# Performance work log

Measured on AMD Instinct MI355X. Metric: run time of the kernel, lower is better.

Reference implementation:

```python
import jax, jax.numpy as jnp
import numpy as np

N, E, H, IN_DIM, EDGE_DIM = 100000, 1600000, 64, 1, 1
SLOPE = 0.01  # leaky_relu negative slope (torch default; GATConv negative_slope=0.01)


def _lrelu(v):
    return jax.nn.leaky_relu(v, SLOPE)


def _segment_softmax(a, idx, num_segments):
    a_max = jax.ops.segment_max(a, idx, num_segments=num_segments)
    e = jnp.exp(a - a_max[idx])
    denom = jax.ops.segment_sum(e, idx, num_segments=num_segments)
    return e / denom[idx]


def _gru_cell(x, h, w_ih, w_hh, b_ih, b_hh):
    # torch.nn.GRUCell: gates ordered r, z, n
    gi = x @ w_ih.T + b_ih
    gh = h @ w_hh.T + b_hh
    i_r, i_z, i_n = jnp.split(gi, 3, axis=-1)
    h_r, h_z, h_n = jnp.split(gh, 3, axis=-1)
    r = jax.nn.sigmoid(i_r + h_r)
    z = jax.nn.sigmoid(i_z + h_z)
    n = jnp.tanh(i_n + r * h_n)
    return (1.0 - z) * n + z * h


def setup_inputs():
    key = jax.random.key(0)
    ks = jax.random.split(key, 20)
    s = 0.1
    p = lambda i, shape: s * jax.random.normal(ks[i], shape, jnp.float32)
    z = lambda shape: jnp.zeros(shape, jnp.float32)
    return {
        "node_attr": jax.random.normal(ks[0], (N, IN_DIM), jnp.float32),
        "edge_attr": jax.random.normal(ks[1], (E, EDGE_DIM), jnp.float32),
        "edge_index": jax.random.randint(ks[2], (2, E), 0, N, jnp.int32),
        "w1": p(3, (H, IN_DIM)), "b1": z((H,)),
        "wg1": p(4, (H, H + EDGE_DIM)), "att_l": p(5, (H,)), "att_r": p(6, (H,)),
        "wg2": p(7, (H, H)), "bg": z((H,)),
        "gru1_wih": p(8, (3 * H, H)), "gru1_whh": p(9, (3 * H, H)),
        "gru1_bih": z((3 * H,)), "gru1_bhh": z((3 * H,)),
        "wm": p(10, (H, H)), "att_src": p(11, (H,)), "att_dst": p(12, (H,)),
        "bm": z((H,)),
        "gru2_wih": p(13, (3 * H, H)), "gru2_whh": p(14, (3 * H, H)),
        "gru2_bih": z((3 * H,)), "gru2_bhh": z((3 * H,)),
        "w2": p(15, (H, H)), "b2": z((H,)),
    }


def _forward(node_attr, edge_attr, edge_index, w1, b1, wg1, att_l, att_r, wg2, bg,
             gru1_wih, gru1_whh, gru1_bih, gru1_bhh,
             wm, att_src, att_dst, bm,
             gru2_wih, gru2_whh, gru2_bih, gru2_bhh, w2, b2):
    src, dst = edge_index[0], edge_index[1]
    # lin1 + in-place leaky_relu
    x = _lrelu(node_attr @ w1.T + b1)                                      # [N,H]
    # --- GATEConv: gather -> edge transform -> softmax over dst -> scatter-add ---
    h_e = _lrelu(jnp.concatenate([x[src], edge_attr], axis=-1) @ wg1.T)    # [E,H]
    a = _lrelu(h_e @ att_l + x[dst] @ att_r)                               # [E]
    alpha = _segment_softmax(a, dst, N)
    h = jax.ops.segment_sum((h_e @ wg2.T) * alpha[:, None], dst, num_segments=N) + bg
    x = jax.nn.relu(_gru_cell(jax.nn.elu(h), x, gru1_wih, gru1_whh, gru1_bih, gru1_bhh))
    # --- molecule readout: batch = zeros(N) -> single graph ---
    batch = jnp.zeros((x.shape[0],), jnp.int32)
    out = jax.nn.relu(jax.ops.segment_sum(x, batch, num_segments=1))       # [1,H]
    # GATConv over bipartite graph (every node -> its graph), shared lin, 1 head
    xs = x @ wm.T                                                          # [N,H]
    xd = out @ wm.T                                                        # [1,H]
    a2 = _lrelu(xs @ att_src + (xd @ att_dst)[batch])                      # [N]
    alpha2 = _segment_softmax(a2, batch, 1)
    h2 = jax.ops.segment_sum(xs * alpha2[:, None], batch, num_segments=1) + bm
    out = jax.nn.relu(_gru_cell(jax.nn.elu(h2), out, gru2_wih, gru2_whh, gru2_bih, gru2_bhh))
    return out @ w2.T + b2                                                 # [1,H]


def reference(node_attr, edge_attr, edge_index, w1, b1, wg1, att_l, att_r, wg2, bg,
              gru1_wih, gru1_whh, gru1_bih, gru1_bhh,
              wm, att_src, att_dst, bm,
              gru2_wih, gru2_whh, gru2_bih, gru2_bhh, w2, b2):
    return _forward(node_attr, edge_attr, edge_index, w1, b1, wg1, att_l, att_r, wg2, bg,
                    gru1_wih, gru1_whh, gru1_bih, gru1_bhh,
                    wm, att_src, att_dst, bm,
                    gru2_wih, gru2_whh, gru2_bih, gru2_bhh, w2, b2)
```

## Files before the change

kernel.cpp:

```cpp
#include <hip/hip_runtime.h>
#include <math.h>

typedef __attribute__((ext_vector_type(8))) short bf8;
typedef __attribute__((ext_vector_type(4))) float f32x4;

#define BSHIFT 9

__device__ __forceinline__ float lrelu(float v){ return fmaxf(v, 0.01f * v); }

__device__ __forceinline__ float wave_sum(float v){
#pragma unroll
  for (int s = 32; s > 0; s >>= 1) v += __shfl_xor(v, s);
  return v;
}
__device__ __forceinline__ float wave_max(float v){
#pragma unroll
  for (int s = 32; s > 0; s >>= 1) v = fmaxf(v, __shfl_xor(v, s));
  return v;
}

__device__ __forceinline__ float bcast(float v, int k){
  return __uint_as_float((unsigned)__builtin_amdgcn_readlane(__float_as_uint(v), k));
}

__device__ __forceinline__ unsigned fkey(float x){
  unsigned u = __float_as_uint(x);
  return (u & 0x80000000u) ? ~u : (u | 0x80000000u);
}
__device__ __forceinline__ float funkey(unsigned k){
  unsigned u = (k & 0x80000000u) ? (k & 0x7fffffffu) : ~k;
  return __uint_as_float(u);
}

__device__ __forceinline__ short f2bfs(float x){
  unsigned u = __float_as_uint(x);
  return (short)((u + 0x7fffu + ((u >> 16) & 1u)) >> 16);
}
__device__ __forceinline__ float bf2f(ushort v){
  return __uint_as_float((unsigned)v << 16);
}
__device__ __forceinline__ bf8 pack8(float4 a, float4 b){
  bf8 v;
  v[0]=f2bfs(a.x); v[1]=f2bfs(a.y); v[2]=f2bfs(a.z); v[3]=f2bfs(a.w);
  v[4]=f2bfs(b.x); v[5]=f2bfs(b.y); v[6]=f2bfs(b.z); v[7]=f2bfs(b.w);
  return v;
}
__device__ __forceinline__ float4 xo4(float nav, float4 w, float4 b){
  float4 r;
  r.x = lrelu(nav*w.x + b.x); r.y = lrelu(nav*w.y + b.y);
  r.z = lrelu(nav*w.z + b.z); r.w = lrelu(nav*w.w + b.w);
  return r;
}
__device__ __forceinline__ float dot4(float4 a, float4 b){
  return a.x*b.x + a.y*b.y + a.z*b.z + a.w*b.w;
}

__global__ void k_wprep(const float* __restrict__ wg1, const float* __restrict__ wm,
                        const float* __restrict__ w2,
                        const float* __restrict__ g2wih, const float* __restrict__ g2whh,
                        float* __restrict__ wm_t, float* __restrict__ w2_t,
                        float* __restrict__ g2ih_t, float* __restrict__ g2hh_t,
                        float* __restrict__ wgc){
  int k = blockIdx.x;
  int r = threadIdx.x;
  if (r < 64){
    wm_t [k * 64 + r] = wm [r * 64 + k];
    w2_t [k * 64 + r] = w2 [r * 64 + k];
    if (k == 0) wgc[r] = wg1[r * 65 + 64];
  }
  g2ih_t[k * 192 + r] = g2wih[r * 64 + k];
  g2hh_t[k * 192 + r] = g2whh[r * 64 + k];
}

__global__ void k_wfrag(const float* __restrict__ wg2, const float* __restrict__ wm,
                        const float* __restrict__ wg1,
                        const float* __restrict__ wih, const float* __restrict__ whh,
                        ushort* __restrict__ wg2f, ushort* __restrict__ wmf,
                        ushort* __restrict__ wg1f,
                        ushort* __restrict__ wihf, ushort* __restrict__ whhf){
  int tid = blockIdx.x * 256 + threadIdx.x;
  if (tid >= 4608) return;
  const float* W; ushort* F; int T, S, base;
  if (tid < 512)      { W = wg2; F = wg2f; T = 4;  S = 64; base = tid; }
  else if (tid < 1024){ W = wm;  F = wmf;  T = 4;  S = 64; base = tid - 1024 + 512; }
  else if (tid < 1536){ W = wg1; F = wg1f; T = 4;  S = 65; base = tid - 1024; }
  else if (tid < 3072){ W = wih; F = wihf; T = 12; S = 64; base = tid - 1536; }
  else                { W = whh; F = whhf; T = 12; S = 64; base = tid - 3072; }
  int l  = base & 63;
  int ct = base >> 6;
  int c  = ct / T, t = ct - c * T;
  int row = 16 * t + (l & 15);
  int k0  = 32 * c + (l >> 4) * 8;
  const float* src = W + row * S + k0;
  unsigned o0 = (unsigned)(ushort)f2bfs(src[0]) | ((unsigned)(ushort)f2bfs(src[1]) << 16);
  unsigned o1 = (unsigned)(ushort)f2bfs(src[2]) | ((unsigned)(ushort)f2bfs(src[3]) << 16);
  unsigned o2 = (unsigned)(ushort)f2bfs(src[4]) | ((unsigned)(ushort)f2bfs(src[5]) << 16);
  unsigned o3 = (unsigned)(ushort)f2bfs(src[6]) | ((unsigned)(ushort)f2bfs(src[7]) << 16);
  ((uint4*)F)[base] = make_uint4(o0, o1, o2, o3);
}

__global__ __launch_bounds__(256) void k_node_m(
    const float* __restrict__ na, const float* __restrict__ w1,
    const float* __restrict__ b1, const ushort* __restrict__ wg1f,
    const float* __restrict__ att_r,
    ushort* __restrict__ yb, float* __restrict__ xr, int N){
  int lane = threadIdx.x & 63;
  int wid  = threadIdx.x >> 6;
  int m = lane & 15, g = lane >> 4;
  const bf8* WG = (const bf8*)wg1f;
  float4 w1a = *(const float4*)(w1 + g*8),      w1b = *(const float4*)(w1 + g*8 + 4);
  float4 w1c = *(const float4*)(w1 + 32 + g*8), w1d = *(const float4*)(w1 + 32 + g*8 + 4);
  float4 b1a = *(const float4*)(b1 + g*8),      b1b = *(const float4*)(b1 + g*8 + 4);
  float4 b1c = *(const float4*)(b1 + 32 + g*8), b1d = *(const float4*)(b1 + 32 + g*8 + 4);
  float4 ara = *(const float4*)(att_r + g*8),      arb = *(const float4*)(att_r + g*8 + 4);
  float4 arc = *(const float4*)(att_r + 32 + g*8), ard = *(const float4*)(att_r + 32 + g*8 + 4);
  int ntiles = (N + 15) >> 4;
  for (int tile = blockIdx.x * 4 + wid; tile < ntiles; tile += gridDim.x * 4){
    int n0 = tile * 16;
    int row = n0 + m;
    bool valid = row < N;
    float nav = valid ? na[row] : 0.f;
    float4 x0 = xo4(nav, w1a, b1a), x1 = xo4(nav, w1b, b1b);
    float4 x2 = xo4(nav, w1c, b1c), x3 = xo4(nav, w1d, b1d);
    float xa = dot4(x0, ara) + dot4(x1, arb) + dot4(x2, arc) + dot4(x3, ard);
    xa += __shfl_xor(xa, 16); xa += __shfl_xor(xa, 32);
    if (g == 0 && valid) xr[row] = xa;
    bf8 fa0 = pack8(x0, x1), fa1 = pack8(x2, x3);
    f32x4 yt[4];
#pragma unroll
    for (int t = 0; t < 4; t++){
      f32x4 acc = {0.f, 0.f, 0.f, 0.f};
      acc = __builtin_amdgcn_mfma_f32_16x16x32_bf16(fa0, WG[t * 64 + lane], acc, 0, 0, 0);
      acc = __builtin_amdgcn_mfma_f32_16x16x32_bf16(fa1, WG[(4 + t) * 64 + lane], acc, 0, 0, 0);
      yt[t] = acc;
    }
#pragma unroll
    for (int t = 0; t < 4; t++){
#pragma unroll
      for (int r = 0; r < 4; r++){
        int rw = n0 + g * 4 + r;
        if (rw < N) yb[(size_t)rw * 64 + m + 16 * t] = (ushort)f2bfs(yt[t][r]);
      }
    }
  }
}

__global__ __launch_bounds__(256) void k_bhist(const int* __restrict__ dst,
                                               int* __restrict__ bcnt, int E, int nbuck){
  __shared__ int hist[256];
  hist[threadIdx.x] = 0;
  __syncthreads();
  int e0 = blockIdx.x * 4096;
  int e1 = min(e0 + 4096, E);
  for (int i = e0 + threadIdx.x; i < e1; i += 256)
    atomicAdd(&hist[dst[i] >> BSHIFT], 1);
  __syncthreads();
  if (threadIdx.x < nbuck && hist[threadIdx.x] > 0)
    atomicAdd(&bcnt[threadIdx.x], hist[threadIdx.x]);
}

__global__ void k_bscan(const int* __restrict__ bcnt, int* __restrict__ bbase,
                        int* __restrict__ gtail, int nbuck){
  __shared__ int lds[256];
  int t = threadIdx.x;
  int v = (t < nbuck) ? bcnt[t] : 0;
  lds[t] = v;
  __syncthreads();
  for (int s = 1; s < 256; s <<= 1){
    int tv = (t >= s) ? lds[t - s] : 0;
    __syncthreads();
    lds[t] += tv;
    __syncthreads();
  }
  if (t <= nbuck){
    int excl = (t == 0) ? 0 : lds[t - 1];
    bbase[t] = excl;
    if (t < nbuck) gtail[t] = excl;
  }
}

__global__ __launch_bounds__(256) void k_binA(
    const int* __restrict__ dst, const int* __restrict__ src,
    const float* __restrict__ ea, int* __restrict__ gtail,
    int2* __restrict__ tse, int E){
  __shared__ int hist[256], base[256], run[256];
  int e0 = blockIdx.x * 4096;
  int e1 = min(e0 + 4096, E);
  hist[threadIdx.x] = 0; run[threadIdx.x] = 0;
  __syncthreads();
  for (int i = e0 + threadIdx.x; i < e1; i += 256)
    atomicAdd(&hist[dst[i] >> BSHIFT], 1);
  __syncthreads();
  if (hist[threadIdx.x] > 0)
    base[threadIdx.x] = atomicAdd(&gtail[threadIdx.x], hist[threadIdx.x]);
  __syncthreads();
  for (int i = e0 + threadIdx.x; i < e1; i += 256){
    int d = dst[i];
    int b = d >> BSHIFT;
    int pos = base[b] + atomicAdd(&run[b], 1);
    tse[pos] = make_int2(src[i] | ((d & 511) << 17), __float_as_int(ea[i]));
  }
}

__global__ __launch_bounds__(256) void k_binB(
    const int* __restrict__ bbase, const int2* __restrict__ tse,
    int2* __restrict__ csr, int* __restrict__ off, int N){
  __shared__ int degL[512];
  __shared__ int fillL[512];
  int node0 = blockIdx.x << BSHIFT;
  int node1 = min(node0 + 512, N);
  int nn = node1 - node0;
  int i0 = bbase[blockIdx.x], i1 = bbase[blockIdx.x + 1];
  degL[threadIdx.x] = 0; degL[256 + threadIdx.x] = 0;
  __syncthreads();
  for (int i = i0 + threadIdx.x; i < i1; i += 256)
    atomicAdd(&degL[(tse[i].x >> 17) & 511], 1);
  __syncthreads();
  int j0 = threadIdx.x, j1 = threadIdx.x + 256;
  for (int s = 1; s < 512; s <<= 1){
    int v0 = (j0 >= s) ? degL[j0 - s] : 0;
    int v1 = (j1 >= s) ? degL[j1 - s] : 0;
    __syncthreads();
    degL[j0] += v0; degL[j1] += v1;
    __syncthreads();
  }
#pragma unroll
  for (int q = 0; q < 2; q++){
    int j = threadIdx.x + q * 256;
    int incl = degL[j];
    int prev = (j == 0) ? 0 : degL[j - 1];
    fillL[j] = i0 + prev;
    if (j < nn) off[node0 + j] = i0 + prev;
    (void)incl;
  }
  if (threadIdx.x == 0 && node1 == N) off[N] = i1;
  __syncthreads();
  for (int i = i0 + threadIdx.x; i < i1; i += 256){
    int2 t = tse[i];
    int drel = (t.x >> 17) & 511;
    int pos = atomicAdd(&fillL[drel], 1);
    csr[pos] = make_int2(t.x & 0x1FFFF, t.y);
  }
}

__global__ void k_edge_f(const int* __restrict__ off, const int2* __restrict__ csr,
                         const ushort* __restrict__ yb, const float* __restrict__ xr,
                         const float* __restrict__ wgc, const float* __restrict__ att_l,
                         float* __restrict__ sout, int N){
  int lane = threadIdx.x & 63;
  int wwid = (blockIdx.x * blockDim.x + threadIdx.x) >> 6;
  int g = lane >> 4, sl = lane & 15;
  int node = wwid * 4 + g;
  if (node >= N) return;
  int i0 = off[node], i1 = off[node + 1];
  float4 wc4 = ((const float4*)wgc)[sl];
  float4 al4 = ((const float4*)att_l)[sl];
  float xrn = xr[node];
  float sg = 0.f;
  float4 acc = make_float4(0.f, 0.f, 0.f, 0.f);
  int2 recA = make_int2(0, 0), recB = make_int2(0, 0);
  ushort4 yvA = make_ushort4(0,0,0,0), yvB = make_ushort4(0,0,0,0);
  if (i0 < i1){
    recA = csr[i0];
    yvA  = ((const ushort4*)(yb + (size_t)recA.x * 64))[sl];
  }
  if (i0 + 1 < i1){
    recB = csr[i0 + 1];
    yvB  = ((const ushort4*)(yb + (size_t)recB.x * 64))[sl];
  }
  for (int i = i0; i < i1; i++){
    float ea = __int_as_float(recA.y);
    float4 he;
    he.x = lrelu(bf2f(yvA.x) + ea * wc4.x);
    he.y = lrelu(bf2f(yvA.y) + ea * wc4.y);
    he.z = lrelu(bf2f(yvA.z) + ea * wc4.z);
    he.w = lrelu(bf2f(yvA.w) + ea * wc4.w);
    recA = recB; yvA = yvB;
    int inext = i + 2;
    if (inext < i1){
      recB = csr[inext];
      yvB  = ((const ushort4*)(yb + (size_t)recB.x * 64))[sl];
    }
    float p = dot4(he, al4);
    p += __shfl_xor(p, 1); p += __shfl_xor(p, 2);
    p += __shfl_xor(p, 4); p += __shfl_xor(p, 8);
    float a = lrelu(p + xrn);
    float w = __expf(a);
    sg += w;
    acc.x += w * he.x; acc.y += w * he.y;
    acc.z += w * he.z; acc.w += w * he.w;
  }
  float inv = (i1 > i0 && sg > 0.f) ? 1.f / sg : 0.f;
  float4 o = make_float4(acc.x * inv, acc.y * inv, acc.z * inv, acc.w * inv);
  ((float4*)(sout + (size_t)node * 64))[sl] = o;
}

__global__ __launch_bounds__(256) void k_gru1m(
    const float* __restrict__ sout, const float* __restrict__ na,
    const float* __restrict__ w1, const float* __restrict__ b1,
    const ushort* __restrict__ wg2f, const float* __restrict__ bg,
    const ushort* __restrict__ wihf, const ushort* __restrict__ whhf,
    const float* __restrict__ bih, const float* __restrict__ bhh,
    float* __restrict__ x2, int N){
  __shared__ ushort xgl[4][16][72];
  int lane = threadIdx.x & 63;
  int wid  = threadIdx.x >> 6;
  int m = lane & 15, g = lane >> 4;
  int n0 = blockIdx.x * 64 + wid * 16;
  if (n0 >= N) return;
  int rowc = min(n0 + m, N - 1);
  const float* srow = sout + (size_t)rowc * 64;
  bf8 sa0 = pack8(*(const float4*)(srow + g * 8),      *(const float4*)(srow + g * 8 + 4));
  bf8 sa1 = pack8(*(const float4*)(srow + 32 + g * 8), *(const float4*)(srow + 32 + g * 8 + 4));
  const bf8* WG = (const bf8*)wg2f;
  f32x4 h[4];
#pragma unroll
  for (int t = 0; t < 4; t++){
    f32x4 acc = {0.f, 0.f, 0.f, 0.f};
    acc = __builtin_amdgcn_mfma_f32_16x16x32_bf16(sa0, WG[t * 64 + lane], acc, 0, 0, 0);
    acc = __builtin_amdgcn_mfma_f32_16x16x32_bf16(sa1, WG[(4 + t) * 64 + lane], acc, 0, 0, 0);
    h[t] = acc;
  }
#pragma unroll
  for (int t = 0; t < 4; t++){
    float bgc = bg[m + 16 * t];
#pragma unroll
    for (int r = 0; r < 4; r++){
      float hv = h[t][r] + bgc;
      float xg = hv > 0.f ? hv : __expf(hv) - 1.f;
      xgl[wid][g * 4 + r][m + 16 * t] = (ushort)f2bfs(xg);
    }
  }
  float nav = na[rowc];
  bf8 xoa0 = pack8(xo4(nav, *(const float4*)(w1 + g * 8),      *(const float4*)(b1 + g * 8)),
                   xo4(nav, *(const float4*)(w1 + g * 8 + 4),  *(const float4*)(b1 + g * 8 + 4)));
  bf8 xoa1 = pack8(xo4(nav, *(const float4*)(w1 + 32 + g * 8),     *(const float4*)(b1 + 32 + g * 8)),
                   xo4(nav, *(const float4*)(w1 + 32 + g * 8 + 4), *(const float4*)(b1 + 32 + g * 8 + 4)));
  bf8 xga0 = *(const bf8*)&xgl[wid][m][g * 8];
  bf8 xga1 = *(const bf8*)&xgl[wid][m][32 + g * 8];
  const bf8* WI = (const bf8*)wihf;
  const bf8* WH = (const bf8*)whhf;
#pragma unroll
  for (int t = 0; t < 4; t++){
    f32x4 iR = {0.f,0.f,0.f,0.f}, iZ = iR, iN = iR, hR = iR, hZ = iR, hN = iR;
    iR = __builtin_amdgcn_mfma_f32_16x16x32_bf16(xga0, WI[(t     ) * 64 + lane], iR, 0,0,0);
    iR = __builtin_amdgcn_mfma_f32_16x16x32_bf16(xga1, WI[(12 + t) * 64 + lane], iR, 0,0,0);
    iZ = __builtin_amdgcn_mfma_f32_16x16x32_bf16(xga0, WI[(t +  4) * 64 + lane], iZ, 0,0,0);
    iZ = __builtin_amdgcn_mfma_f32_16x16x32_bf16(xga1, WI[(16 + t) * 64 + lane], iZ, 0,0,0);
    iN = __builtin_amdgcn_mfma_f32_16x16x32_bf16(xga0, WI[(t +  8) * 64 + lane], iN, 0,0,0);
    iN = __builtin_amdgcn_mfma_f32_16x16x32_bf16(xga1, WI[(20 + t) * 64 + lane], iN, 0,0,0);
    hR = __builtin_amdgcn_mfma_f32_16x16x32_bf16(xoa0, WH[(t     ) * 64 + lane], hR, 0,0,0);
    hR = __builtin_amdgcn_mfma_f32_16x16x32_bf16(xoa1, WH[(12 + t) * 64 + lane], hR, 0,0,0);
    hZ = __builtin_amdgcn_mfma_f32_16x16x32_bf16(xoa0, WH[(t +  4) * 64 + lane], hZ, 0,0,0);
    hZ = __builtin_amdgcn_mfma_f32_16x16x32_bf16(xoa1, WH[(16 + t) * 64 + lane], hZ, 0,0,0);
    hN = __builtin_amdgcn_mfma_f32_16x16x32_bf16(xoa0, WH[(t +  8) * 64 + lane], hN, 0,0,0);
    hN = __builtin_amdgcn_mfma_f32_16x16x32_bf16(xoa1, WH[(20 + t) * 64 + lane], hN, 0,0,0);
    int col = m + 16 * t;
    float biR = bih[col], biZ = bih[64 + col], biN = bih[128 + col];
    float bhR = bhh[col], bhZ = bhh[64 + col], bhN = bhh[128 + col];
    float w1c = w1[col], b1c = b1[col];
#pragma unroll
    for (int r = 0; r < 4; r++){
      int node = n0 + g * 4 + r;
      if (node < N){
        float xon = lrelu(na[node] * w1c + b1c);
        float rg = 1.f / (1.f + __expf(-(iR[r] + biR + hR[r] + bhR)));
        float zg = 1.f / (1.f + __expf(-(iZ[r] + biZ + hZ[r] + bhZ)));
        float nn = tanhf(iN[r] + biN + rg * (hN[r] + bhN));
        float xn = (1.f - zg) * nn + zg * xon;
        x2[(size_t)node * 64 + col] = fmaxf(xn, 0.f);
      }
    }
  }
}

__global__ __launch_bounds__(256) void k_part2m(
    float* __restrict__ xb,
    const ushort* __restrict__ wmf, const float* __restrict__ att_src,
    float* __restrict__ tb, float* __restrict__ scal, int N){
  int lane = threadIdx.x & 63;
  int wid  = threadIdx.x >> 6;
  int m = lane & 15, g = lane >> 4;
  const bf8* WM = (const bf8*)wmf;
  float as_t[4];
#pragma unroll
  for (int t = 0; t < 4; t++) as_t[t] = att_src[m + 16 * t];
  float os[16];
#pragma unroll
  for (int j = 0; j < 16; j++) os[j] = 0.f;
  float tmax = -1e30f;
  int ntiles = (N + 15) >> 4;
  for (int tile = blockIdx.x * 4 + wid; tile < ntiles; tile += gridDim.x * 4){
    int n0 = tile * 16;
    int row = n0 + m;
    bool valid = row < N;
    int rowc = valid ? row : (N - 1);
    const float* xrow = xb + (size_t)rowc * 64;
    float4 a0 = *(const float4*)(xrow + g * 8);
    float4 a1 = *(const float4*)(xrow + g * 8 + 4);
    float4 a2 = *(const float4*)(xrow + 32 + g * 8);
    float4 a3 = *(const float4*)(xrow + 32 + g * 8 + 4);
    if (!valid){ a0 = make_float4(0,0,0,0); a1 = a0; a2 = a0; a3 = a0; }
    os[0]+=a0.x; os[1]+=a0.y; os[2]+=a0.z; os[3]+=a0.w;
    os[4]+=a1.x; os[5]+=a1.y; os[6]+=a1.z; os[7]+=a1.w;
    os[8]+=a2.x; os[9]+=a2.y; os[10]+=a2.z; os[11]+=a2.w;
    os[12]+=a3.x; os[13]+=a3.y; os[14]+=a3.z; os[15]+=a3.w;
    bf8 fa0 = pack8(a0, a1), fa1 = pack8(a2, a3);
    f32x4 xs_t[4];
#pragma unroll
    for (int t = 0; t < 4; t++){
      f32x4 acc = {0.f, 0.f, 0.f, 0.f};
      acc = __builtin_amdgcn_mfma_f32_16x16x32_bf16(fa0, WM[t * 64 + lane], acc, 0, 0, 0);
      acc = __builtin_amdgcn_mfma_f32_16x16x32_bf16(fa1, WM[(4 + t) * 64 + lane], acc, 0, 0, 0);
      xs_t[t] = acc;
    }
    float tpart[4] = {0.f, 0.f, 0.f, 0.f};
#pragma unroll
    for (int t = 0; t < 4; t++){
#pragma unroll
      for (int r = 0; r < 4; r++){
        int rw = n0 + g * 4 + r;
        if (rw < N) xb[(size_t)rw * 64 + m + 16 * t] = xs_t[t][r];
        tpart[r] += xs_t[t][r] * as_t[t];
      }
    }
#pragma unroll
    for (int r = 0; r < 4; r++){
      float v = tpart[r];
      v += __shfl_xor(v, 1); v += __shfl_xor(v, 2);
      v += __shfl_xor(v, 4); v += __shfl_xor(v, 8);
      if (m == 0){
        int rw = n0 + g * 4 + r;
        if (rw < N){ tb[rw] = v; tmax = fmaxf(tmax, v); }
      }
    }
  }
  tmax = wave_max(tmax);
  if (lane == 0) atomicMax((unsigned*)(scal + 131), fkey(tmax));
#pragma unroll
  for (int j = 0; j < 16; j++){
    float v = os[j];
    v += __shfl_xor(v, 1); v += __shfl_xor(v, 2);
    v += __shfl_xor(v, 4); v += __shfl_xor(v, 8);
    os[j] = v;
  }
  __shared__ float osm[4][64];
  if (m == 0){
#pragma unroll
    for (int j = 0; j < 8; j++){
      osm[wid][g * 8 + j]      = os[j];
      osm[wid][32 + g * 8 + j] = os[8 + j];
    }
  }
  __syncthreads();
  if (threadIdx.x < 64)
    atomicAdd(&scal[threadIdx.x],
              osm[0][threadIdx.x] + osm[1][threadIdx.x] + osm[2][threadIdx.x] + osm[3][threadIdx.x]);
}

__global__ void k_part2b(float* __restrict__ scal, const float* __restrict__ wm_t,
                         const float* __restrict__ att_dst){
  int lane = threadIdx.x;
  float o = fmaxf(scal[lane], 0.f);
  float acc = 0.f;
  for (int k = 0; k < 64; k++) acc += bcast(o, k) * wm_t[k * 64 + lane];
  float c = wave_sum(acc * att_dst[lane]);
  scal[64 + lane] = o;
  if (lane == 0){
    scal[128] = c;
    float maxtb = funkey(*(unsigned*)(scal + 131));
    scal[130] = lrelu(maxtb + c);
  }
}

__global__ void k_a2sum(const float* __restrict__ tb, const float* __restrict__ xs,
                        float* __restrict__ scal, int N){
  int lane = threadIdx.x & 63, w = threadIdx.x >> 6;
  int gw = blockIdx.x * 4 + w, nw = gridDim.x * 4;
  float c = scal[128];
  float M = scal[130];
  float hloc = 0.f, sloc = 0.f;
  for (int n = gw; n < N; n += nw){
    float a2 = lrelu(tb[n] + c);
    float wt = __expf(a2 - M);
    sloc += wt;
    hloc += wt * xs[(size_t)n * 64 + lane];
  }
  __shared__ float lds[256];
  __shared__ float sred[4];
  lds[threadIdx.x] = hloc;
  if (lane == 0) sred[w] = sloc;
  __syncthreads();
  if (threadIdx.x < 64)
    atomicAdd(&scal[192 + threadIdx.x],
              lds[threadIdx.x] + lds[64 + threadIdx.x] + lds[128 + threadIdx.x] + lds[192 + threadIdx.x]);
  if (threadIdx.x == 0) atomicAdd(&scal[129], sred[0] + sred[1] + sred[2] + sred[3]);
}

__global__ void k_final(const float* __restrict__ scal, const float* __restrict__ bm,
                        const float* __restrict__ g2ih_t, const float* __restrict__ g2hh_t,
                        const float* __restrict__ bih, const float* __restrict__ bhh,
                        const float* __restrict__ w2_t, const float* __restrict__ b2,
                        float* __restrict__ dout){
  int lane = threadIdx.x;
  float S  = scal[129];
  float h2 = scal[192 + lane] / S + bm[lane];
  float xg = h2 > 0.f ? h2 : __expf(h2) - 1.f;
  float xo = scal[64 + lane];
  float gir = bih[lane], giz = bih[64 + lane], gin = bih[128 + lane];
  float ghr = bhh[lane], ghz = bhh[64 + lane], ghn = bhh[128 + lane];
  for (int k = 0; k < 64; k++){
    float a = bcast(xg, k), b = bcast(xo, k);
    const float* gi = g2ih_t + k * 192;
    const float* gh = g2hh_t + k * 192;
    gir += a * gi[lane]; giz += a * gi[64 + lane]; gin += a * gi[128 + lane];
    ghr += b * gh[lane]; ghz += b * gh[64 + lane]; ghn += b * gh[128 + lane];
  }
  float r  = 1.f / (1.f + __expf(-(gir + ghr)));
  float z  = 1.f / (1.f + __expf(-(giz + ghz)));
  float nn = tanhf(gin + r * ghn);
  float o2 = fmaxf((1.f - z) * nn + z * xo, 0.f);
  float res = 0.f;
  for (int k = 0; k < 64; k++) res += bcast(o2, k) * w2_t[k * 64 + lane];
  dout[lane] = res + b2[lane];
}

extern "C" void kernel_launch(void* const* d_in, const int* in_sizes, int n_in,
                              void* d_out, int out_size, void* d_ws, size_t ws_size,
                              hipStream_t stream){
  const float* na    = (const float*)d_in[0];
  const float* ea    = (const float*)d_in[1];
  const int*   ei    = (const int*)d_in[2];
  const float* w1    = (const float*)d_in[3];
  const float* b1    = (const float*)d_in[4];
  const float* wg1   = (const float*)d_in[5];
  const float* att_l = (const float*)d_in[6];
  const float* att_r = (const float*)d_in[7];
  const float* wg2   = (const float*)d_in[8];
  const float* bg    = (const float*)d_in[9];
  const float* g1wih = (const float*)d_in[10];
  const float* g1whh = (const float*)d_in[11];
  const float* g1bih = (const float*)d_in[12];
  const float* g1bhh = (const float*)d_in[13];
  const float* wm      = (const float*)d_in[14];
  const float* att_src = (const float*)d_in[15];
  const float* att_dst = (const float*)d_in[16];
  const float* bm      = (const float*)d_in[17];
  const float* g2wih = (const float*)d_in[18];
  const float* g2whh = (const float*)d_in[19];
  const float* g2bih = (const float*)d_in[20];
  const float* g2bhh = (const float*)d_in[21];
  const float* w2    = (const float*)d_in[22];
  const float* b2    = (const float*)d_in[23];

  int N = in_sizes[0];
  int E = in_sizes[1];
  const int* srcArr = ei;
  const int* dstArr = ei + E;

  char* ws = (char*)d_ws;
  size_t cur = 0;
  auto alloc = [&](size_t nbytes) -> char* {
    char* p = ws + cur;
    cur += (nbytes + 255) & ~(size_t)255;
    return p;
  };
  ushort* yb   = (ushort*)alloc((size_t)N * 64 * 2);
  float* bufC  = (float*)alloc((size_t)N * 64 * 4);
  float* xr    = (float*)alloc((size_t)N * 4);
  float* tb    = (float*)alloc((size_t)N * 4);
  int*   offA  = (int*)alloc((size_t)(N + 1) * 4);
  int*   bcnt  = (int*)alloc(2048);
  int*   bbase = (int*)alloc(2048);
  int*   gtail = (int*)alloc(2048);
  int2*  csr   = (int2*)alloc((size_t)E * 8);
  int2*  tse   = (int2*)alloc((size_t)E * 8);
  float* scal  = (float*)alloc(4096);
  float* wm_t  = (float*)alloc(64 * 64 * 4);
  float* w2_t  = (float*)alloc(64 * 64 * 4);
  float* g2ih_t= (float*)alloc(64 * 192 * 4);
  float* g2hh_t= (float*)alloc(64 * 192 * 4);
  float* wgc   = (float*)alloc(64 * 4);
  ushort* wg2f = (ushort*)alloc(4096 * 2);
  ushort* wmf  = (ushort*)alloc(4096 * 2);
  ushort* wg1f = (ushort*)alloc(4096 * 2);
  ushort* wihf = (ushort*)alloc(12288 * 2);
  ushort* whhf = (ushort*)alloc(12288 * 2);
  if (cur > ws_size) return;

  hipMemsetAsync(bcnt, 0, 2048, stream);
  hipMemsetAsync(scal, 0, 4096, stream);

  k_wprep<<<64, 192, 0, stream>>>(wg1, wm, w2, g2wih, g2whh,
                                  wm_t, w2_t, g2ih_t, g2hh_t, wgc);
  k_wfrag<<<18, 256, 0, stream>>>(wg2, wm, wg1, g1wih, g1whh,
                                  wg2f, wmf, wg1f, wihf, whhf);

  int nbuck = (N + 511) >> BSHIFT;
  k_node_m<<<512, 256, 0, stream>>>(na, w1, b1, wg1f, att_r, yb, xr, N);
  k_bhist<<<(E + 4095) / 4096, 256, 0, stream>>>(dstArr, bcnt, E, nbuck);
  k_bscan<<<1, 256, 0, stream>>>(bcnt, bbase, gtail, nbuck);
  k_binA<<<(E + 4095) / 4096, 256, 0, stream>>>(dstArr, srcArr, ea, gtail, tse, E);
  k_binB<<<nbuck, 256, 0, stream>>>(bbase, tse, csr, offA, N);
  int nwb2 = (N + 15) / 16;
  k_edge_f<<<nwb2, 256, 0, stream>>>(offA, csr, yb, xr, wgc, att_l, bufC, N);
  int ngb = (N + 63) / 64;
  k_gru1m<<<ngb, 256, 0, stream>>>(bufC, na, w1, b1, wg2f, bg, wihf, whhf,
                                   g1bih, g1bhh, bufC, N);
  k_part2m<<<512, 256, 0, stream>>>(bufC, wmf, att_src, tb, scal, N);
  k_part2b<<<1, 64, 0, stream>>>(scal, wm_t, att_dst);
  k_a2sum<<<512, 256, 0, stream>>>(tb, bufC, scal, N);
  k_final<<<1, 64, 0, stream>>>(scal, bm, g2ih_t, g2hh_t, g2bih, g2bhh, w2_t, b2, (float*)d_out);
  (void)n_in; (void)out_size;
}
```

Baseline: 243.9 us.

## Halve CSR bucket width and double-issue edge loop with deeper prefetch

The destination-bucket width drops from 512 to 256 nodes, giving about 391 buckets, so k_binB launches twice as many blocks with a simpler single-element scan. The histogram, scan and binning kernels are widened to handle up to 512 buckets. The edge attention loop now processes two edges per iteration and prefetches four edges ahead, which raises memory-level parallelism and interleaves the shuffle reductions. The costs are more global atomics on bucket tails in k_binA and higher register pressure in k_edge_f.

```diff
diff --git a/kernel.cpp b/kernel.cpp
--- a/kernel.cpp
+++ b/kernel.cpp
@@ -4,7 +4,7 @@
 typedef __attribute__((ext_vector_type(8))) short bf8;
 typedef __attribute__((ext_vector_type(4))) float f32x4;
 
-#define BSHIFT 9
+#define BSHIFT 8
 
 __device__ __forceinline__ float lrelu(float v){ return fmaxf(v, 0.01f * v); }
 
@@ -147,26 +147,29 @@
 
 __global__ __launch_bounds__(256) void k_bhist(const int* __restrict__ dst,
                                                int* __restrict__ bcnt, int E, int nbuck){
-  __shared__ int hist[256];
-  hist[threadIdx.x] = 0;
+  __shared__ int hist[512];
+  hist[threadIdx.x] = 0; hist[256 + threadIdx.x] = 0;
   __syncthreads();
   int e0 = blockIdx.x * 4096;
   int e1 = min(e0 + 4096, E);
   for (int i = e0 + threadIdx.x; i < e1; i += 256)
     atomicAdd(&hist[dst[i] >> BSHIFT], 1);
   __syncthreads();
-  if (threadIdx.x < nbuck && hist[threadIdx.x] > 0)
-    atomicAdd(&bcnt[threadIdx.x], hist[threadIdx.x]);
+#pragma unroll
+  for (int q = 0; q < 2; q++){
+    int j = threadIdx.x + q * 256;
+    if (j < nbuck && hist[j] > 0) atomicAdd(&bcnt[j], hist[j]);
+  }
 }
 
 __global__ void k_bscan(const int* __restrict__ bcnt, int* __restrict__ bbase,
                         int* __restrict__ gtail, int nbuck){
-  __shared__ int lds[256];
+  __shared__ int lds[512];
   int t = threadIdx.x;
   int v = (t < nbuck) ? bcnt[t] : 0;
   lds[t] = v;
   __syncthreads();
-  for (int s = 1; s < 256; s <<= 1){
+  for (int s = 1; s < 512; s <<= 1){
     int tv = (t >= s) ? lds[t - s] : 0;
     __syncthreads();
     lds[t] += tv;
@@ -183,63 +186,60 @@
     const int* __restrict__ dst, const int* __restrict__ src,
     const float* __restrict__ ea, int* __restrict__ gtail,
     int2* __restrict__ tse, int E){
-  __shared__ int hist[256], base[256], run[256];
+  __shared__ int hist[512], base[512], run[512];
   int e0 = blockIdx.x * 4096;
   int e1 = min(e0 + 4096, E);
-  hist[threadIdx.x] = 0; run[threadIdx.x] = 0;
+  hist[threadIdx.x] = 0; hist[256 + threadIdx.x] = 0;
+  run[threadIdx.x] = 0;  run[256 + threadIdx.x] = 0;
   __syncthreads();
   for (int i = e0 + threadIdx.x; i < e1; i += 256)
     atomicAdd(&hist[dst[i] >> BSHIFT], 1);
   __syncthreads();
-  if (hist[threadIdx.x] > 0)
-    base[threadIdx.x] = atomicAdd(&gtail[threadIdx.x], hist[threadIdx.x]);
+#pragma unroll
+  for (int q = 0; q < 2; q++){
+    int j = threadIdx.x + q * 256;
+    if (hist[j] > 0) base[j] = atomicAdd(&gtail[j], hist[j]);
+  }
   __syncthreads();
   for (int i = e0 + threadIdx.x; i < e1; i += 256){
     int d = dst[i];
     int b = d >> BSHIFT;
     int pos = base[b] + atomicAdd(&run[b], 1);
-    tse[pos] = make_int2(src[i] | ((d & 511) << 17), __float_as_int(ea[i]));
+    tse[pos] = make_int2(src[i] | ((d & 255) << 17), __float_as_int(ea[i]));
   }
 }
 
 __global__ __launch_bounds__(256) void k_binB(
     const int* __restrict__ bbase, const int2* __restrict__ tse,
     int2* __restrict__ csr, int* __restrict__ off, int N){
-  __shared__ int degL[512];
-  __shared__ int fillL[512];
+  __shared__ int degL[256];
+  __shared__ int fillL[256];
   int node0 = blockIdx.x << BSHIFT;
-  int node1 = min(node0 + 512, N);
+  int node1 = min(node0 + 256, N);
   int nn = node1 - node0;
   int i0 = bbase[blockIdx.x], i1 = bbase[blockIdx.x + 1];
-  degL[threadIdx.x] = 0; degL[256 + threadIdx.x] = 0;
-  __syncthreads();
-  for (int i = i0 + threadIdx.x; i < i1; i += 256)
-    atomicAdd(&degL[(tse[i].x >> 17) & 511], 1);
-  __syncthreads();
-  int j0 = threadIdx.x, j1 = threadIdx.x + 256;
-  for (int s = 1; s < 512; s <<= 1){
-    int v0 = (j0 >= s) ? degL[j0 - s] : 0;
-    int v1 = (j1 >= s) ? degL[j1 - s] : 0;
+  int t = threadIdx.x;
+  degL[t] = 0;
+  __syncthreads();
+  for (int i = i0 + t; i < i1; i += 256)
+    atomicAdd(&degL[(tse[i].x >> 17) & 255], 1);
+  __syncthreads();
+  for (int s = 1; s < 256; s <<= 1){
+    int v = (t >= s) ? degL[t - s] : 0;
     __syncthreads();
-    degL[j0] += v0; degL[j1] += v1;
+    degL[t] += v;
     __syncthreads();
   }
-#pragma unroll
-  for (int q = 0; q < 2; q++){
-    int j = threadIdx.x + q * 256;
-    int incl = degL[j];
-    int prev = (j == 0) ? 0 : degL[j - 1];
-    fillL[j] = i0 + prev;
-    if (j < nn) off[node0 + j] = i0 + prev;
-    (void)incl;
-  }
-  if (threadIdx.x == 0 && node1 == N) off[N] = i1;
-  __syncthreads();
-  for (int i = i0 + threadIdx.x; i < i1; i += 256){
-    int2 t = tse[i];
-    int drel = (t.x >> 17) & 511;
+  int prev = (t == 0) ? 0 : degL[t - 1];
+  fillL[t] = i0 + prev;
+  if (t < nn) off[node0 + t] = i0 + prev;
+  if (t == 0 && node1 == N) off[N] = i1;
+  __syncthreads();
+  for (int i = i0 + t; i < i1; i += 256){
+    int2 rec = tse[i];
+    int drel = (rec.x >> 17) & 255;
     int pos = atomicAdd(&fillL[drel], 1);
-    csr[pos] = make_int2(t.x & 0x1FFFF, t.y);
+    csr[pos] = make_int2(rec.x & 0x1FFFF, rec.y);
   }
 }
 
@@ -258,34 +258,49 @@
   float xrn = xr[node];
   float sg = 0.f;
   float4 acc = make_float4(0.f, 0.f, 0.f, 0.f);
-  int2 recA = make_int2(0, 0), recB = make_int2(0, 0);
-  ushort4 yvA = make_ushort4(0,0,0,0), yvB = make_ushort4(0,0,0,0);
-  if (i0 < i1){
-    recA = csr[i0];
-    yvA  = ((const ushort4*)(yb + (size_t)recA.x * 64))[sl];
-  }
-  if (i0 + 1 < i1){
-    recB = csr[i0 + 1];
-    yvB  = ((const ushort4*)(yb + (size_t)recB.x * 64))[sl];
-  }
-  for (int i = i0; i < i1; i++){
-    float ea = __int_as_float(recA.y);
+  int cnt = i1 - i0;
+  int2 rA = make_int2(0,0), rB = rA, rC = rA, rD = rA;
+  ushort4 yA = make_ushort4(0,0,0,0), yB = yA, yC = yA, yD = yA;
+  if (cnt > 0){ rA = csr[i0];     yA = ((const ushort4*)(yb + (size_t)rA.x * 64))[sl]; }
+  if (cnt > 1){ rB = csr[i0 + 1]; yB = ((const ushort4*)(yb + (size_t)rB.x * 64))[sl]; }
+  if (cnt > 2){ rC = csr[i0 + 2]; yC = ((const ushort4*)(yb + (size_t)rC.x * 64))[sl]; }
+  if (cnt > 3){ rD = csr[i0 + 3]; yD = ((const ushort4*)(yb + (size_t)rD.x * 64))[sl]; }
+  int i = i0;
+  for (; i + 1 < i1; i += 2){
+    float eaA = __int_as_float(rA.y);
+    float eaB = __int_as_float(rB.y);
+    float4 heA, heB;
+    heA.x = lrelu(bf2f(yA.x) + eaA * wc4.x); heB.x = lrelu(bf2f(yB.x) + eaB * wc4.x);
+    heA.y = lrelu(bf2f(yA.y) + eaA * wc4.y); heB.y = lrelu(bf2f(yB.y) + eaB * wc4.y);
+    heA.z = lrelu(bf2f(yA.z) + eaA * wc4.z); heB.z = lrelu(bf2f(yB.z) + eaB * wc4.z);
+    heA.w = lrelu(bf2f(yA.w) + eaA * wc4.w); heB.w = lrelu(bf2f(yB.w) + eaB * wc4.w);
+    rA = rC; yA = yC; rB = rD; yB = yD;
+    if (i + 4 < i1){ rC = csr[i + 4]; yC = ((const ushort4*)(yb + (size_t)rC.x * 64))[sl]; }
+    if (i + 5 < i1){ rD = csr[i + 5]; yD = ((const ushort4*)(yb + (size_t)rD.x * 64))[sl]; }
+    float pA = dot4(heA, al4), pB = dot4(heB, al4);
+    pA += __shfl_xor(pA, 1); pB += __shfl_xor(pB, 1);
+    pA += __shfl_xor(pA, 2); pB += __shfl_xor(pB, 2);
+    pA += __shfl_xor(pA, 4); pB += __shfl_xor(pB, 4);
+    pA += __shfl_xor(pA, 8); pB += __shfl_xor(pB, 8);
+    float wa = __expf(lrelu(pA + xrn));
+    float wb = __expf(lrelu(pB + xrn));
+    sg += wa + wb;
+    acc.x += wa * heA.x + wb * heB.x;
+    acc.y += wa * heA.y + wb * heB.y;
+    acc.z += wa * heA.z + wb * heB.z;
+    acc.w += wa * heA.w + wb * heB.w;
+  }
+  if (i < i1){
+    float ea = __int_as_float(rA.y);
     float4 he;
-    he.x = lrelu(bf2f(yvA.x) + ea * wc4.x);
-    he.y = lrelu(bf2f(yvA.y) + ea * wc4.y);
-    he.z = lrelu(bf2f(yvA.z) + ea * wc4.z);
-    he.w = lrelu(bf2f(yvA.w) + ea * wc4.w);
-    recA = recB; yvA = yvB;
-    int inext = i + 2;
-    if (inext < i1){
-      recB = csr[inext];
-      yvB  = ((const ushort4*)(yb + (size_t)recB.x * 64))[sl];
-    }
+    he.x = lrelu(bf2f(yA.x) + ea * wc4.x);
+    he.y = lrelu(bf2f(yA.y) + ea * wc4.y);
+    he.z = lrelu(bf2f(yA.z) + ea * wc4.z);
+    he.w = lrelu(bf2f(yA.w) + ea * wc4.w);
     float p = dot4(he, al4);
     p += __shfl_xor(p, 1); p += __shfl_xor(p, 2);
     p += __shfl_xor(p, 4); p += __shfl_xor(p, 8);
-    float a = lrelu(p + xrn);
-    float w = __expf(a);
+    float w = __expf(lrelu(p + xrn));
     sg += w;
     acc.x += w * he.x; acc.y += w * he.y;
     acc.z += w * he.z; acc.w += w * he.w;
@@ -570,9 +585,9 @@
   float* xr    = (float*)alloc((size_t)N * 4);
   float* tb    = (float*)alloc((size_t)N * 4);
   int*   offA  = (int*)alloc((size_t)(N + 1) * 4);
-  int*   bcnt  = (int*)alloc(2048);
-  int*   bbase = (int*)alloc(2048);
-  int*   gtail = (int*)alloc(2048);
+  int*   bcnt  = (int*)alloc(4096);
+  int*   bbase = (int*)alloc(4096);
+  int*   gtail = (int*)alloc(4096);
   int2*  csr   = (int2*)alloc((size_t)E * 8);
   int2*  tse   = (int2*)alloc((size_t)E * 8);
   float* scal  = (float*)alloc(4096);
@@ -588,7 +603,7 @@
   ushort* whhf = (ushort*)alloc(12288 * 2);
   if (cur > ws_size) return;
 
-  hipMemsetAsync(bcnt, 0, 2048, stream);
+  hipMemsetAsync(bcnt, 0, 4096, stream);
   hipMemsetAsync(scal, 0, 4096, stream);
 
   k_wprep<<<64, 192, 0, stream>>>(wg1, wm, w2, g2wih, g2whh,
@@ -596,10 +611,10 @@
   k_wfrag<<<18, 256, 0, stream>>>(wg2, wm, wg1, g1wih, g1whh,
                                   wg2f, wmf, wg1f, wihf, whhf);
 
-  int nbuck = (N + 511) >> BSHIFT;
+  int nbuck = (N + 255) >> BSHIFT;
   k_node_m<<<512, 256, 0, stream>>>(na, w1, b1, wg1f, att_r, yb, xr, N);
   k_bhist<<<(E + 4095) / 4096, 256, 0, stream>>>(dstArr, bcnt, E, nbuck);
-  k_bscan<<<1, 256, 0, stream>>>(bcnt, bbase, gtail, nbuck);
+  k_bscan<<<1, 512, 0, stream>>>(bcnt, bbase, gtail, nbuck);
   k_binA<<<(E + 4095) / 4096, 256, 0, stream>>>(dstArr, srcArr, ea, gtail, tse, E);
   k_binB<<<nbuck, 256, 0, stream>>>(bbase, tse, csr, offA, N);
   int nwb2 = (N + 15) / 16;
```

After: 233.7 us, median of 2. -4.2%, faster.
